# Optimization experiments

Hardware: AMD Instinct MI355X
Metric: run time of the kernel (lower is better)

## Reference

```python
import jax, jax.numpy as jnp
import numpy as np

B, S, D_IN, D_OUT = 4, 2048, 4096, 4096
ALPHA, INSCALE = 0.001, 0.05


def setup_inputs() -> dict:
    key = jax.random.key(0)
    kx, kw = jax.random.split(key)
    x = jax.random.normal(kx, (B, S, D_IN), dtype=jnp.float32)
    # int8 weight in [-127, 126], matching torch.randint(-127, 127, ...)
    weight = jax.random.randint(kw, (D_OUT, D_IN), -127, 127, dtype=jnp.int32).astype(jnp.int8)
    return {
        "x": x,
        "weight": weight,
        "alpha": jnp.float32(ALPHA),
        "inscale": jnp.float32(INSCALE),
    }


def reference(x, weight, alpha, inscale):
    x_shape = x.shape
    xf = x.reshape(-1, x_shape[-1])                        # [M, K]
    # dynamic per-tensor int8 quantization of activations
    q = jnp.clip(jnp.round(xf / inscale), -128, 127).astype(jnp.int8)
    y = jax.lax.dot_general(
        q, weight,
        dimension_numbers=(((1,), (1,)), ((), ())),
        preferred_element_type=jnp.int32,
    )
    # dequant epilogue: scalar alpha scale -> fp32
    y = y.astype(jnp.float32) * alpha
    return y.reshape(*x_shape[:-1], -1)                    # [B, S, N]
```

## Files before the change

kernel.cpp:

```cpp
#include <hip/hip_runtime.h>
#include <hip/hip_bf16.h>
#include <cstdint>


typedef int v4i  __attribute__((ext_vector_type(4)));
typedef int v16i __attribute__((ext_vector_type(16)));

#define BM 128
#define BN 128
#define BK 64
#define NTHREADS 256

__global__ void prep_kernel(const float* __restrict__ x,
                            signed char* __restrict__ q,
                            const int* __restrict__ w32,
                            signed char* __restrict__ w8,
                            const float* __restrict__ inscale_ptr,
                            int nq_threads) {
    const int i = blockIdx.x * blockDim.x + threadIdx.x;
    if (i < nq_threads) {
        const float s = *inscale_ptr;
        float4 f = ((const float4*)x)[i];
        union { signed char c[4]; int v; } u;
        float vals[4] = {f.x, f.y, f.z, f.w};
#pragma unroll
        for (int e = 0; e < 4; ++e) {
            float r = rintf(vals[e] / s);
            r = fminf(fmaxf(r, -128.0f), 127.0f);
            u.c[e] = (signed char)(int)r;
        }
        ((int*)q)[i] = u.v;
    } else {
        const int j = i - nq_threads;
        int4 w = ((const int4*)w32)[j];
        union { signed char c[4]; int v; } u;
        u.c[0] = (signed char)w.x;
        u.c[1] = (signed char)w.y;
        u.c[2] = (signed char)w.z;
        u.c[3] = (signed char)w.w;
        ((int*)w8)[j] = u.v;
    }
}

__device__ __forceinline__ void async16(void* lds, const void* g) {
    __builtin_amdgcn_global_load_lds(
        (const __attribute__((address_space(1))) void*)g,
        (__attribute__((address_space(3))) void*)lds,
        16, 0, 0);
}

__global__ __launch_bounds__(NTHREADS, 4)
void w8a8_gemm(const signed char* __restrict__ A,
               const signed char* __restrict__ Bw,
               float* __restrict__ C,
               const float* __restrict__ alpha_ptr,
               int M, int N, int K) {
    __shared__ signed char lA[BM * BK];
    __shared__ signed char lB[BN * BK];

    const int t    = threadIdx.x;
    const int lane = t & 63;
    const int wave = t >> 6;
    const int wm   = (wave >> 1) * 64;
    const int wn   = (wave & 1) * 64;

    const int tileM = blockIdx.y * BM;
    const int tileN = blockIdx.x * BN;

    const int i0 = t;
    const int i1 = t + NTHREADS;
    const int r0 = i0 >> 2, g0 = (i0 & 3) ^ (r0 & 3);
    const int r1 = i1 >> 2, g1 = (i1 & 3) ^ (r1 & 3);

    const size_t aOff0 = (size_t)(tileM + r0) * K + g0 * 16;
    const size_t aOff1 = (size_t)(tileM + r1) * K + g1 * 16;
    const size_t bOff0 = (size_t)(tileN + r0) * K + g0 * 16;
    const size_t bOff1 = (size_t)(tileN + r1) * K + g1 * 16;

    const int mrow  = lane & 31;
    const int khalf = lane >> 5;

    auto fragAddr = [&](int row, int fg) -> int {
        return (row * 4 + (fg ^ (row & 3))) * 16;
    };

    v16i acc[2][2] = {};

    for (int k0 = 0; k0 < K; k0 += BK) {
        async16(&lA[i0 * 16], A + aOff0 + k0);
        async16(&lA[i1 * 16], A + aOff1 + k0);
        async16(&lB[i0 * 16], Bw + bOff0 + k0);
        async16(&lB[i1 * 16], Bw + bOff1 + k0);
        __syncthreads();

        v4i a[2][2], b[2][2];
#pragma unroll
        for (int s = 0; s < 2; ++s) {
            const int fg = 2 * s + khalf;
#pragma unroll
            for (int im = 0; im < 2; ++im)
                a[im][s] = *(const v4i*)&lA[fragAddr(wm + im * 32 + mrow, fg)];
#pragma unroll
            for (int jn = 0; jn < 2; ++jn)
                b[jn][s] = *(const v4i*)&lB[fragAddr(wn + jn * 32 + mrow, fg)];
        }

#pragma unroll
        for (int s = 0; s < 2; ++s)
#pragma unroll
            for (int im = 0; im < 2; ++im)
#pragma unroll
                for (int jn = 0; jn < 2; ++jn)
                    acc[im][jn] = __builtin_amdgcn_mfma_i32_32x32x32_i8(
                        a[im][s], b[jn][s], acc[im][jn], 0, 0, 0);

        __syncthreads();
    }

    const float alpha = *alpha_ptr;
    const int ccol  = lane & 31;
    const int rquad = (lane >> 5) * 4;
#pragma unroll
    for (int im = 0; im < 2; ++im) {
#pragma unroll
        for (int jn = 0; jn < 2; ++jn) {
            const int baseRow = tileM + wm + im * 32;
            const int col     = tileN + wn + jn * 32 + ccol;
#pragma unroll
            for (int reg = 0; reg < 16; ++reg) {
                const int row = baseRow + (reg & 3) + 8 * (reg >> 2) + rquad;
                C[(size_t)row * N + col] = (float)acc[im][jn][reg] * alpha;
            }
        }
    }
}

extern "C" void kernel_launch(void* const* d_in, const int* in_sizes, int n_in,
                              void* d_out, int out_size, void* d_ws, size_t ws_size,
                              hipStream_t stream) {
    const float* x       = (const float*)d_in[0];
    const int*   w32     = (const int*)d_in[1];
    const float* alpha   = (const float*)d_in[2];
    const float* inscale = (const float*)d_in[3];
    float*       out     = (float*)d_out;

    const int K = 4096;
    const int N = 4096;
    const int M = in_sizes[0] / K;

    signed char* q  = (signed char*)d_ws;
    signed char* w8 = (signed char*)d_ws + (size_t)M * K;

    const int nq_threads = (M * K) / 4;
    const int nw_threads = (N * K) / 4;
    const int total      = nq_threads + nw_threads;
    prep_kernel<<<(total + 255) / 256, 256, 0, stream>>>(x, q, w32, w8, inscale,
                                                         nq_threads);

    dim3 grid(N / BN, M / BM);
    w8a8_gemm<<<grid, NTHREADS, 0, stream>>>(q, w8, out, alpha, M, N, K);
}
```

Measured before the change: 423.9 us.

## Enlarge GEMM tiles to 256x256 with triple-buffered async LDS pipeline

Result: faster. 413.7 us (-2.4%).

```diff
diff --git a/kernel.cpp b/kernel.cpp
--- a/kernel.cpp
+++ b/kernel.cpp
@@ -1,44 +1,47 @@
 #include <hip/hip_runtime.h>
-#include <hip/hip_bf16.h>
 #include <cstdint>
 
 
 typedef int v4i  __attribute__((ext_vector_type(4)));
 typedef int v16i __attribute__((ext_vector_type(16)));
 
-#define BM 128
-#define BN 128
-#define BK 64
-#define NTHREADS 256
+#define BM 256
+#define BN 256
+#define BKB 64
+#define LDS_TILE (BM * BKB)
+#define LDS_BUF  (2 * LDS_TILE)
+#define NBUF 3
 
 __global__ void prep_kernel(const float* __restrict__ x,
                             signed char* __restrict__ q,
                             const int* __restrict__ w32,
                             signed char* __restrict__ w8,
                             const float* __restrict__ inscale_ptr,
-                            int nq_threads) {
-    const int i = blockIdx.x * blockDim.x + threadIdx.x;
-    if (i < nq_threads) {
-        const float s = *inscale_ptr;
-        float4 f = ((const float4*)x)[i];
-        union { signed char c[4]; int v; } u;
-        float vals[4] = {f.x, f.y, f.z, f.w};
+                            int nq, int total) {
+    const float s = *inscale_ptr;
+    const int stride = gridDim.x * blockDim.x;
+    for (int i = blockIdx.x * blockDim.x + threadIdx.x; i < total; i += stride) {
+        if (i < nq) {
+            float4 f = ((const float4*)x)[i];
+            union { signed char c[4]; int v; } u;
+            float vals[4] = {f.x, f.y, f.z, f.w};
 #pragma unroll
-        for (int e = 0; e < 4; ++e) {
-            float r = rintf(vals[e] / s);
-            r = fminf(fmaxf(r, -128.0f), 127.0f);
-            u.c[e] = (signed char)(int)r;
+            for (int e = 0; e < 4; ++e) {
+                float r = rintf(vals[e] / s);
+                r = fminf(fmaxf(r, -128.0f), 127.0f);
+                u.c[e] = (signed char)(int)r;
+            }
+            ((int*)q)[i] = u.v;
+        } else {
+            const int j = i - nq;
+            int4 w = ((const int4*)w32)[j];
+            union { signed char c[4]; int v; } u;
+            u.c[0] = (signed char)w.x;
+            u.c[1] = (signed char)w.y;
+            u.c[2] = (signed char)w.z;
+            u.c[3] = (signed char)w.w;
+            ((int*)w8)[j] = u.v;
         }
-        ((int*)q)[i] = u.v;
-    } else {
-        const int j = i - nq_threads;
-        int4 w = ((const int4*)w32)[j];
-        union { signed char c[4]; int v; } u;
-        u.c[0] = (signed char)w.x;
-        u.c[1] = (signed char)w.y;
-        u.c[2] = (signed char)w.z;
-        u.c[3] = (signed char)w.w;
-        ((int*)w8)[j] = u.v;
     }
 }
 
@@ -49,79 +52,111 @@
         16, 0, 0);
 }
 
-__global__ __launch_bounds__(NTHREADS, 4)
+__global__ __launch_bounds__(512, 2)
 void w8a8_gemm(const signed char* __restrict__ A,
                const signed char* __restrict__ Bw,
                float* __restrict__ C,
                const float* __restrict__ alpha_ptr,
                int M, int N, int K) {
-    __shared__ signed char lA[BM * BK];
-    __shared__ signed char lB[BN * BK];
+    __shared__ signed char lds[NBUF * LDS_BUF];
 
     const int t    = threadIdx.x;
     const int lane = t & 63;
     const int wave = t >> 6;
-    const int wm   = (wave >> 1) * 64;
-    const int wn   = (wave & 1) * 64;
+    const int wm   = (wave >> 2) * 128;
+    const int wn   = (wave & 3) * 64;
 
-    const int tileM = blockIdx.y * BM;
-    const int tileN = blockIdx.x * BN;
+    const int nbx   = N / BN;
+    const int swz   = ((int)blockIdx.x & 7) * ((int)gridDim.x >> 3)
+                    + ((int)blockIdx.x >> 3);
+    const int tileM = (swz / nbx) * BM;
+    const int tileN = (swz % nbx) * BN;
 
-    const int i0 = t;
-    const int i1 = t + NTHREADS;
-    const int r0 = i0 >> 2, g0 = (i0 & 3) ^ (r0 & 3);
-    const int r1 = i1 >> 2, g1 = (i1 & 3) ^ (r1 & 3);
+    const int srow = t >> 2;
+    const int sg   = (t & 3) ^ ((t >> 3) & 3);
+    const size_t aOff0 = (size_t)(tileM + srow)       * K + sg * 16;
+    const size_t aOff1 = (size_t)(tileM + 128 + srow) * K + sg * 16;
+    const size_t bOff0 = (size_t)(tileN + srow)       * K + sg * 16;
+    const size_t bOff1 = (size_t)(tileN + 128 + srow) * K + sg * 16;
+    const int ldst = t * 16;
 
-    const size_t aOff0 = (size_t)(tileM + r0) * K + g0 * 16;
-    const size_t aOff1 = (size_t)(tileM + r1) * K + g1 * 16;
-    const size_t bOff0 = (size_t)(tileN + r0) * K + g0 * 16;
-    const size_t bOff1 = (size_t)(tileN + r1) * K + g1 * 16;
+    auto stageA = [&](int kt, int buf) {
+        const size_t ko = (size_t)kt * BKB;
+        signed char* d = &lds[buf * LDS_BUF];
+        async16(d + ldst,        A + aOff0 + ko);
+        async16(d + 8192 + ldst, A + aOff1 + ko);
+    };
+    auto stageB = [&](int kt, int buf) {
+        const size_t ko = (size_t)kt * BKB;
+        signed char* d = &lds[buf * LDS_BUF + LDS_TILE];
+        async16(d + ldst,        Bw + bOff0 + ko);
+        async16(d + 8192 + ldst, Bw + bOff1 + ko);
+    };
 
     const int mrow  = lane & 31;
     const int khalf = lane >> 5;
+    const int fswz  = (mrow >> 1) & 3;
+    const int offS0 = ((0 + khalf) ^ fswz) * 16;
+    const int offS1 = ((2 + khalf) ^ fswz) * 16;
+    int arow[4], brow[2];
+#pragma unroll
+    for (int im = 0; im < 4; ++im) arow[im] = (wm + im * 32 + mrow) * BKB;
+#pragma unroll
+    for (int jn = 0; jn < 2; ++jn) brow[jn] = LDS_TILE + (wn + jn * 32 + mrow) * BKB;
 
-    auto fragAddr = [&](int row, int fg) -> int {
-        return (row * 4 + (fg ^ (row & 3))) * 16;
+    v16i acc[4][2] = {};
+
+    auto phase = [&](const signed char* cb, int offp) {
+        v4i a[4], b[2];
+#pragma unroll
+        for (int im = 0; im < 4; ++im)
+            a[im] = *(const v4i*)(cb + arow[im] + offp);
+#pragma unroll
+        for (int jn = 0; jn < 2; ++jn)
+            b[jn] = *(const v4i*)(cb + brow[jn] + offp);
+        asm volatile("s_barrier" ::: "memory");
+        __builtin_amdgcn_s_setprio(1);
+#pragma unroll
+        for (int im = 0; im < 4; ++im)
+#pragma unroll
+            for (int jn = 0; jn < 2; ++jn)
+                acc[im][jn] = __builtin_amdgcn_mfma_i32_32x32x32_i8(
+                    a[im], b[jn], acc[im][jn], 0, 0, 0);
+        __builtin_amdgcn_s_setprio(0);
     };
 
-    v16i acc[2][2] = {};
+    stageA(0, 0); stageB(0, 0);
+    stageA(1, 1); stageB(1, 1);
+    asm volatile("s_waitcnt vmcnt(4)" ::: "memory");
+    asm volatile("s_barrier" ::: "memory");
 
-    for (int k0 = 0; k0 < K; k0 += BK) {
-        async16(&lA[i0 * 16], A + aOff0 + k0);
-        async16(&lA[i1 * 16], A + aOff1 + k0);
-        async16(&lB[i0 * 16], Bw + bOff0 + k0);
-        async16(&lB[i1 * 16], Bw + bOff1 + k0);
-        __syncthreads();
+    const int NT = K / BKB;
+    int bc = 0, sb = 2;
+#pragma unroll 1
+    for (int kt = 0; kt < NT; ++kt) {
+        const bool doStage = (kt + 2) < NT;
+        const signed char* cb = &lds[bc * LDS_BUF];
 
-        v4i a[2][2], b[2][2];
-#pragma unroll
-        for (int s = 0; s < 2; ++s) {
-            const int fg = 2 * s + khalf;
-#pragma unroll
-            for (int im = 0; im < 2; ++im)
-                a[im][s] = *(const v4i*)&lA[fragAddr(wm + im * 32 + mrow, fg)];
-#pragma unroll
-            for (int jn = 0; jn < 2; ++jn)
-                b[jn][s] = *(const v4i*)&lB[fragAddr(wn + jn * 32 + mrow, fg)];
-        }
+        if (doStage) stageA(kt + 2, sb);
+        phase(cb, offS0);
+        asm volatile("s_barrier" ::: "memory");
 
-#pragma unroll
-        for (int s = 0; s < 2; ++s)
-#pragma unroll
-            for (int im = 0; im < 2; ++im)
-#pragma unroll
-                for (int jn = 0; jn < 2; ++jn)
-                    acc[im][jn] = __builtin_amdgcn_mfma_i32_32x32x32_i8(
-                        a[im][s], b[jn][s], acc[im][jn], 0, 0, 0);
+        if (doStage) stageB(kt + 2, sb);
+        phase(cb, offS1);
 
-        __syncthreads();
+        if (doStage) asm volatile("s_waitcnt vmcnt(4)" ::: "memory");
+        else         asm volatile("s_waitcnt vmcnt(0)" ::: "memory");
+        asm volatile("s_barrier" ::: "memory");
+
+        bc = (bc == NBUF - 1) ? 0 : bc + 1;
+        sb = (sb == NBUF - 1) ? 0 : sb + 1;
     }
 
     const float alpha = *alpha_ptr;
     const int ccol  = lane & 31;
-    const int rquad = (lane >> 5) * 4;
+    const int rquad = khalf * 4;
 #pragma unroll
-    for (int im = 0; im < 2; ++im) {
+    for (int im = 0; im < 4; ++im) {
 #pragma unroll
         for (int jn = 0; jn < 2; ++jn) {
             const int baseRow = tileM + wm + im * 32;
@@ -151,12 +186,10 @@
     signed char* q  = (signed char*)d_ws;
     signed char* w8 = (signed char*)d_ws + (size_t)M * K;
 
-    const int nq_threads = (M * K) / 4;
-    const int nw_threads = (N * K) / 4;
-    const int total      = nq_threads + nw_threads;
-    prep_kernel<<<(total + 255) / 256, 256, 0, stream>>>(x, q, w32, w8, inscale,
-                                                         nq_threads);
+    const int nq    = (M * K) / 4;
+    const int total = nq + (N * K) / 4;
+    prep_kernel<<<2048, 256, 0, stream>>>(x, q, w32, w8, inscale, nq, total);
 
-    dim3 grid(N / BN, M / BM);
-    w8a8_gemm<<<grid, NTHREADS, 0, stream>>>(q, w8, out, alpha, M, N, K);
+    dim3 grid((M / BM) * (N / BN));
+    w8a8_gemm<<<grid, 512, 0, stream>>>(q, w8, out, alpha, M, N, K);
 }
```
